# Kernel tuning notes

Measured on AMD Instinct MI355X. Metric: run time of the kernel, lower is better.

The kernel has to match this reference:

```python
import jax, jax.numpy as jnp
import numpy as np

B, C, J, T = 32, 128, 24, 128
Q, K = 6, 1024
EPS = 1e-10


def setup_inputs() -> dict:
    key = jax.random.key(0)
    k1, k2 = jax.random.split(key)
    x = jax.random.normal(k1, (B, C, J, T), dtype=jnp.float32)
    codebooks = jax.random.normal(k2, (Q, K, C), dtype=jnp.float32)
    return {"x": x, "codebooks": codebooks}


def reference(x, codebooks):
    """Residual VQ over 2D joint-temporal tokens.
    x: (B, C, J, T); codebooks: (Q, K, C).
    Returns (quantized_out (B,C,J,T), all_indices (B,J,T,Q), loss scalar, perplexity scalar).
    """
    b, c, j, t = x.shape
    q, k, _ = codebooks.shape
    # preprocess: (B, C, J, T) -> (B*J*T, C)
    xf = jnp.transpose(x, (0, 2, 3, 1)).reshape(-1, c)
    m = xf.shape[0]

    def step(carry, codebook):
        residual, q_out = carry
        # squared L2 distances (M, K)
        d = (jnp.sum(residual * residual, axis=-1, keepdims=True)
             - 2.0 * (residual @ codebook.T)
             + jnp.sum(codebook * codebook, axis=-1))
        idx = jnp.argmin(d, axis=-1)                       # (M,)
        xd = codebook[idx]                                 # dequantize (M, C)
        # commitment loss: mse(x, x_d.detach())
        loss = jnp.mean((residual - jax.lax.stop_gradient(xd)) ** 2)
        # perplexity from code usage histogram
        counts = jax.ops.segment_sum(jnp.ones((m,), xf.dtype), idx, num_segments=k)
        p = counts / m
        perp = jnp.exp(-jnp.sum(p * jnp.log(p + EPS)))
        # straight-through estimator
        quant = residual + jax.lax.stop_gradient(xd - residual)
        # residual = residual - quantized.detach(); quantized_out += quantized
        new_res = residual - jax.lax.stop_gradient(quant)
        return (new_res, q_out + quant), (idx, loss, perp)

    init = (xf, jnp.zeros_like(xf))
    (_, q_out), (idxs, losses, perps) = jax.lax.scan(step, init, codebooks)

    quantized_out = jnp.transpose(q_out.reshape(b, j, t, c), (0, 3, 1, 2))
    all_indices = jnp.transpose(idxs, (1, 0)).reshape(b, j, t, q)
    return quantized_out, all_indices, jnp.mean(losses), jnp.mean(perps)
```

## Files before the change

kernel.cpp:

```cpp
#include <hip/hip_runtime.h>

typedef __attribute__((ext_vector_type(8))) short short8v;
typedef __attribute__((ext_vector_type(4))) float f32x4;

#define B_ 32
#define C_ 128
#define J_ 24
#define T_ 128
#define Q_ 6
#define K_ 1024
#define JT (J_*T_)
#define M_ (B_*JT)
#define NBLK 768

#define OUT_QUANT 0
#define OUT_IDX   12582912
#define OUT_LOSS  13172736
#define OUT_PERP  13172737

#define TAU_S 0.01f

__device__ __forceinline__ unsigned short f2bf(float f) {
    unsigned int u = __float_as_uint(f);
    u = (u + 0x7FFFu + ((u >> 16) & 1u)) >> 16;
    return (unsigned short)u;
}
__device__ __forceinline__ float bf2f(unsigned short h) {
    return __uint_as_float(((unsigned int)h) << 16);
}

__device__ __forceinline__ void gload16(const void* g, void* lds) {
    __builtin_amdgcn_global_load_lds(
        (const __attribute__((address_space(1))) void*)g,
        (__attribute__((address_space(3))) void*)lds, 16, 0, 0);
}

__global__ __launch_bounds__(256) void c2_kernel(const float* __restrict__ cb,
                                                 float* __restrict__ c2) {
    int wave = (blockIdx.x * blockDim.x + threadIdx.x) >> 6;
    int lane = threadIdx.x & 63;
    if (wave >= Q_ * K_) return;
    const float2 v = reinterpret_cast<const float2*>(cb + (size_t)wave * C_)[lane];
    float s = v.x * v.x + v.y * v.y;
    #pragma unroll
    for (int off = 32; off; off >>= 1) s += __shfl_down(s, off, 64);
    if (lane == 0) c2[wave] = s;
}

__global__ __launch_bounds__(256) void cbtile_kernel(const float* __restrict__ cb,
                                                     unsigned short* __restrict__ cbt) {
    int i = blockIdx.x * 256 + threadIdx.x;
    if (i >= Q_ * 32 * 1024) return;
    int q = i >> 15;
    int rem = i & 32767;
    int tau = rem >> 10;
    int slot = rem & 1023;
    int part = slot >> 9;
    int ks = (slot >> 7) & 3;
    int nt = (slot >> 6) & 1;
    int r6 = slot & 63;
    int a = (r6 >> 4) & 3;
    int b3 = (r6 >> 3) & 1;
    int low3 = r6 & 7;
    int c4 = (b3 << 3) | (low3 ^ a);
    int code = tau * 32 + nt * 16 + c4;
    const float* src = cb + ((size_t)q * K_ + code) * C_ + ks * 32 + a * 8;
    short8v v;
    #pragma unroll
    for (int j = 0; j < 8; ++j) {
        float f = src[j];
        unsigned short hh = f2bf(f);
        v[j] = (part == 0) ? (short)hh : (short)f2bf(f - bf2f(hh));
    }
    *(short8v*)(cbt + (size_t)i * 8) = v;
}

__global__ __launch_bounds__(256) void transpose_kernel(const float* __restrict__ x,
                                                        float* __restrict__ res) {
    __shared__ float tile[32][33];
    const int tx = threadIdx.x & 31, ty = threadIdx.x >> 5;
    const int jt0 = blockIdx.x * 32;
    const int c0 = blockIdx.y * 32;
    const int b = blockIdx.z;
    const float* xb = x + ((size_t)b * C_ + c0) * JT + jt0;
    #pragma unroll
    for (int i = 0; i < 4; ++i) {
        int cc = ty + 8 * i;
        tile[cc][tx] = xb[(size_t)cc * JT + tx];
    }
    __syncthreads();
    float* rb = res + ((size_t)b * JT + jt0) * C_ + c0;
    #pragma unroll
    for (int i = 0; i < 4; ++i) {
        int jj = ty + 8 * i;
        rb[(size_t)jj * C_ + tx] = tile[tx][jj];
    }
}

__global__ __launch_bounds__(256, 3) void vq_fused_kernel(
        float* __restrict__ res,
        const float* __restrict__ cb,
        const unsigned short* __restrict__ cbt,
        const float* __restrict__ c2g,
        int* __restrict__ idxws, int* __restrict__ counts,
        float* __restrict__ partials) {
    __shared__ __attribute__((aligned(16))) unsigned short bsA[8192];
    __shared__ __attribute__((aligned(16))) unsigned short bsB[8192];
    __shared__ __attribute__((aligned(16))) unsigned short bsC[8192];
    __shared__ int idx_lds[128];
    __shared__ int nflag[4];
    __shared__ int flagl[4][32];
    __shared__ float wsum[4];
    __shared__ __attribute__((aligned(16))) float rowbuf[4][128];

    const int t = threadIdx.x;
    const int w = t >> 6, l = t & 63;
    const int la = l >> 4;
    const int lc = l & 15;
    const int rowbase = blockIdx.x * 128 + w * 32;
    const int lb = la * 256 + (l & 8) * 16 + (((l & 7) ^ la) * 16);

    float rres[64];
    #pragma unroll
    for (int mf = 0; mf < 2; ++mf) {
        const float* ap = res + (size_t)(rowbase + mf * 16 + lc) * C_ + la * 8;
        #pragma unroll
        for (int ks = 0; ks < 4; ++ks) {
            float4 f0 = *(const float4*)(ap + ks * 32);
            float4 f1 = *(const float4*)(ap + ks * 32 + 4);
            rres[mf * 32 + ks * 8 + 0] = f0.x; rres[mf * 32 + ks * 8 + 1] = f0.y;
            rres[mf * 32 + ks * 8 + 2] = f0.z; rres[mf * 32 + ks * 8 + 3] = f0.w;
            rres[mf * 32 + ks * 8 + 4] = f1.x; rres[mf * 32 + ks * 8 + 5] = f1.y;
            rres[mf * 32 + ks * 8 + 6] = f1.z; rres[mf * 32 + ks * 8 + 7] = f1.w;
        }
    }

#define STAGE(base_, tau_, buf_) { \
        const unsigned short* sp = (base_) + (size_t)(tau_) * 8192 + w * 2048 + l * 8; \
        char* dp = ((char*)(buf_)) + w * 4096; \
        gload16(sp, dp); \
        gload16(sp + 512, dp + 1024); \
        gload16(sp + 1024, dp + 2048); \
        gload16(sp + 1536, dp + 3072); \
    }

    for (int q = 0; q < Q_; ++q) {
        const int qk0 = q * K_;
        const unsigned short* cbase = cbt + (size_t)q * (32 * 8192);
        if (l == 0) nflag[w] = 0;

        float c2r0 = c2g[qk0 + lc];
        float c2r1 = c2g[qk0 + 16 + lc];

        STAGE(cbase, 0, bsA)
        STAGE(cbase, 1, bsB)

        short8v ah[2][4], al[2][4];
        #pragma unroll
        for (int mf = 0; mf < 2; ++mf) {
            #pragma unroll
            for (int ks = 0; ks < 4; ++ks) {
                short8v vh, vl;
                #pragma unroll
                for (int j = 0; j < 8; ++j) {
                    float v = rres[mf * 32 + ks * 8 + j];
                    unsigned short hh = f2bf(v);
                    vh[j] = (short)hh;
                    vl[j] = (short)f2bf(v - bf2f(hh));
                }
                ah[mf][ks] = vh;
                al[mf][ks] = vl;
            }
        }

        float bs[2][4], bs2[2][4];
        int bi[2][4];
        #pragma unroll
        for (int mf = 0; mf < 2; ++mf)
            #pragma unroll
            for (int rg = 0; rg < 4; ++rg) {
                bs[mf][rg] = -3.4e38f; bs2[mf][rg] = -3.4e38f; bi[mf][rg] = 0;
            }

        asm volatile("s_waitcnt vmcnt(4)" ::: "memory");
        __builtin_amdgcn_s_barrier();
        float c2n0 = -0.5f * c2r0;
        float c2n1 = -0.5f * c2r1;

        const char* bcur = (const char*)bsA;
        const char* bnx1 = (const char*)bsB;
        const char* bnx2 = (const char*)bsC;

        for (int tau = 0; tau < 32; ++tau) {
            if (tau < 31) {
                c2r0 = c2g[qk0 + (tau + 1) * 32 + lc];
                c2r1 = c2g[qk0 + (tau + 1) * 32 + 16 + lc];
            }
            if (tau < 30) STAGE(cbase, tau + 2, (void*)bnx2)

            #pragma unroll
            for (int nt = 0; nt < 2; ++nt) {
                const int code = tau * 32 + nt * 16 + lc;
                const float cinit = nt ? c2n1 : c2n0;
                f32x4 acc0 = {cinit, cinit, cinit, cinit};
                f32x4 acc1 = acc0;
                #pragma unroll
                for (int ks = 0; ks < 4; ++ks) {
                    const char* bb = bcur + ks * 2048 + nt * 1024 + lb;
                    const short8v bh = *(const short8v*)(bb);
                    const short8v bl = *(const short8v*)(bb + 8192);
                    acc0 = __builtin_amdgcn_mfma_f32_16x16x32_bf16(ah[0][ks], bh, acc0, 0, 0, 0);
                    acc0 = __builtin_amdgcn_mfma_f32_16x16x32_bf16(al[0][ks], bh, acc0, 0, 0, 0);
                    acc0 = __builtin_amdgcn_mfma_f32_16x16x32_bf16(ah[0][ks], bl, acc0, 0, 0, 0);
                    acc1 = __builtin_amdgcn_mfma_f32_16x16x32_bf16(ah[1][ks], bh, acc1, 0, 0, 0);
                    acc1 = __builtin_amdgcn_mfma_f32_16x16x32_bf16(al[1][ks], bh, acc1, 0, 0, 0);
                    acc1 = __builtin_amdgcn_mfma_f32_16x16x32_bf16(ah[1][ks], bl, acc1, 0, 0, 0);
                }
#define UPD(A, mf, rg) { \
                float v = A[rg]; \
                bs2[mf][rg] = fmaxf(bs2[mf][rg], fminf(bs[mf][rg], v)); \
                bool gt = v > bs[mf][rg]; \
                bs[mf][rg] = fmaxf(bs[mf][rg], v); \
                bi[mf][rg] = gt ? code : bi[mf][rg]; }
                UPD(acc0, 0, 0) UPD(acc0, 0, 1) UPD(acc0, 0, 2) UPD(acc0, 0, 3)
                UPD(acc1, 1, 0) UPD(acc1, 1, 1) UPD(acc1, 1, 2) UPD(acc1, 1, 3)
#undef UPD
            }

            if (tau < 30) {
                asm volatile("s_waitcnt vmcnt(4)" ::: "memory");
            } else if (tau == 30) {
                asm volatile("s_waitcnt vmcnt(2)" ::: "memory");
            } else {
                asm volatile("s_waitcnt vmcnt(0)" ::: "memory");
            }
            __builtin_amdgcn_s_barrier();
            c2n0 = -0.5f * c2r0;
            c2n1 = -0.5f * c2r1;
            const char* tmp = bcur; bcur = bnx1; bnx1 = bnx2; bnx2 = tmp;
        }

        #pragma unroll
        for (int mf = 0; mf < 2; ++mf) {
            #pragma unroll
            for (int rg = 0; rg < 4; ++rg) {
                float s1 = bs[mf][rg], s2 = bs2[mf][rg];
                int i1 = bi[mf][rg];
                #pragma unroll
                for (int off = 1; off < 16; off <<= 1) {
                    float os1 = __shfl_xor(s1, off);
                    float os2 = __shfl_xor(s2, off);
                    int oi1 = __shfl_xor(i1, off);
                    float ns2 = fmaxf(fmaxf(s2, os2), fminf(s1, os1));
                    if (os1 > s1 || (os1 == s1 && oi1 < i1)) { s1 = os1; i1 = oi1; }
                    s2 = ns2;
                }
                if (lc == 0) {
                    const int rr = mf * 16 + la * 4 + rg;
                    idx_lds[w * 32 + rr] = i1;
                    if (s1 - s2 < TAU_S) {
                        int p = atomicAdd(&nflag[w], 1);
                        flagl[w][p] = rr;
                    }
                }
            }
        }

        {
            const int nf = nflag[w];
            for (int f = 0; f < nf; ++f) {
                const int rr = flagl[w][f];
                const int mfr = rr >> 4, r16 = rr & 15;
                if (lc == r16) {
                    #pragma unroll
                    for (int ks = 0; ks < 4; ++ks) {
                        #pragma unroll
                        for (int j = 0; j < 8; ++j)
                            rowbuf[w][la * 8 + ks * 32 + j] =
                                (mfr == 0) ? rres[ks * 8 + j] : rres[32 + ks * 8 + j];
                    }
                }
                asm volatile("s_waitcnt lgkmcnt(0)" ::: "memory");
                __builtin_amdgcn_sched_barrier(0);
                const float4* rf4 = (const float4*)&rowbuf[w][0];
                double bdd = 1e300;
                int bk = 0;
                for (int kk = 0; kk < 16; ++kk) {
                    const int k = l + kk * 64;
                    const float4* bp4 = (const float4*)(cb + ((size_t)qk0 + k) * C_);
                    double s = 0.0;
                    for (int c4 = 0; c4 < 32; ++c4) {
                        float4 bv = bp4[c4];
                        float4 rv = rf4[c4];
                        double d0 = (double)rv.x - (double)bv.x; s = fma(d0, d0, s);
                        double d1 = (double)rv.y - (double)bv.y; s = fma(d1, d1, s);
                        double d2 = (double)rv.z - (double)bv.z; s = fma(d2, d2, s);
                        double d3 = (double)rv.w - (double)bv.w; s = fma(d3, d3, s);
                    }
                    if (s < bdd || (s == bdd && k < bk)) { bdd = s; bk = k; }
                }
                #pragma unroll
                for (int off = 1; off < 64; off <<= 1) {
                    double od = __shfl_xor(bdd, off);
                    int ok = __shfl_xor(bk, off);
                    if (od < bdd || (od == bdd && ok < bk)) { bdd = od; bk = ok; }
                }
                if (l == 0) idx_lds[w * 32 + rr] = bk;
                asm volatile("s_waitcnt lgkmcnt(0)" ::: "memory");
            }
        }

        if (l < 16) {
            const int k0 = idx_lds[w * 32 + l];
            const int k1 = idx_lds[w * 32 + 16 + l];
            idxws[(size_t)q * M_ + rowbase + l] = k0;
            idxws[(size_t)q * M_ + rowbase + 16 + l] = k1;
            atomicAdd(&counts[qk0 + k0], 1);
            atomicAdd(&counts[qk0 + k1], 1);
        }

        float sq = 0.f;
        #pragma unroll
        for (int mf = 0; mf < 2; ++mf) {
            const int k = idx_lds[w * 32 + mf * 16 + lc];
            const float* cbr = cb + ((size_t)qk0 + k) * C_ + la * 8;
            #pragma unroll
            for (int ks = 0; ks < 4; ++ks) {
                float4 cv0 = *(const float4*)(cbr + ks * 32);
                float4 cv1 = *(const float4*)(cbr + ks * 32 + 4);
                float cvv[8] = {cv0.x, cv0.y, cv0.z, cv0.w, cv1.x, cv1.y, cv1.z, cv1.w};
                #pragma unroll
                for (int j = 0; j < 8; ++j) {
                    float rv = rres[mf * 32 + ks * 8 + j];
                    float cvj = cvv[j];
                    float dd = rv - cvj;
                    sq += dd * dd;
                    rres[mf * 32 + ks * 8 + j] = rv - (rv + (cvj - rv));
                }
            }
        }
        #pragma unroll
        for (int off = 32; off; off >>= 1) sq += __shfl_down(sq, off, 64);
        if (l == 0) wsum[w] = sq;
        __syncthreads();
        if (t == 0) partials[q * NBLK + blockIdx.x] = wsum[0] + wsum[1] + wsum[2] + wsum[3];
        __syncthreads();
    }

    #pragma unroll
    for (int mf = 0; mf < 2; ++mf) {
        float* ap = res + (size_t)(rowbase + mf * 16 + lc) * C_ + la * 8;
        #pragma unroll
        for (int ks = 0; ks < 4; ++ks) {
            float4 f0 = *(const float4*)(ap + ks * 32);
            float4 f1 = *(const float4*)(ap + ks * 32 + 4);
            float4 o0, o1;
            o0.x = f0.x - rres[mf * 32 + ks * 8 + 0];
            o0.y = f0.y - rres[mf * 32 + ks * 8 + 1];
            o0.z = f0.z - rres[mf * 32 + ks * 8 + 2];
            o0.w = f0.w - rres[mf * 32 + ks * 8 + 3];
            o1.x = f1.x - rres[mf * 32 + ks * 8 + 4];
            o1.y = f1.y - rres[mf * 32 + ks * 8 + 5];
            o1.z = f1.z - rres[mf * 32 + ks * 8 + 6];
            o1.w = f1.w - rres[mf * 32 + ks * 8 + 7];
            *(float4*)(ap + ks * 32) = o0;
            *(float4*)(ap + ks * 32 + 4) = o1;
        }
    }
#undef STAGE
}

__global__ __launch_bounds__(256) void scalars_kernel(const float* __restrict__ partials,
                                                      const int* __restrict__ counts,
                                                      float* __restrict__ out) {
    __shared__ float red[256];
    const int t = threadIdx.x;
    float loss_acc = 0.f, perp_acc = 0.f;
    for (int q = 0; q < Q_; ++q) {
        float s = 0.f;
        for (int i = t; i < NBLK; i += 256) s += partials[q * NBLK + i];
        red[t] = s;
        __syncthreads();
        for (int o = 128; o; o >>= 1) {
            if (t < o) red[t] += red[t + o];
            __syncthreads();
        }
        if (t == 0) loss_acc += red[0] / (float)(M_ * C_);
        __syncthreads();
    }
    for (int q = 0; q < Q_; ++q) {
        float s = 0.f;
        for (int k = t; k < K_; k += 256) {
            float p = (float)counts[q * K_ + k] / (float)M_;
            s += p * logf(p + 1e-10f);
        }
        red[t] = s;
        __syncthreads();
        for (int o = 128; o; o >>= 1) {
            if (t < o) red[t] += red[t + o];
            __syncthreads();
        }
        if (t == 0) perp_acc += expf(-red[0]);
        __syncthreads();
    }
    if (t == 0) {
        out[OUT_LOSS] = loss_acc / (float)Q_;
        out[OUT_PERP] = perp_acc / (float)Q_;
    }
}

__global__ __launch_bounds__(256) void finalt_kernel(const float* __restrict__ qout,
                                                     float* __restrict__ out) {
    __shared__ float tile[32][33];
    const int tx = threadIdx.x & 31, ty = threadIdx.x >> 5;
    const int jt0 = blockIdx.x * 32;
    const int c0 = blockIdx.y * 32;
    const int b = blockIdx.z;
    const float* qb = qout + ((size_t)b * JT + jt0) * C_ + c0;
    #pragma unroll
    for (int i = 0; i < 4; ++i) {
        int jj = ty + 8 * i;
        tile[jj][tx] = qb[(size_t)jj * C_ + tx];
    }
    __syncthreads();
    float* ob = out + ((size_t)b * C_ + c0) * JT + jt0;
    #pragma unroll
    for (int i = 0; i < 4; ++i) {
        int cc = ty + 8 * i;
        ob[(size_t)cc * JT + tx] = tile[tx][cc];
    }
}

__global__ __launch_bounds__(256) void idxout_kernel(const int* __restrict__ idxin,
                                                     float* __restrict__ out) {
    int f = blockIdx.x * 256 + threadIdx.x;
    if (f >= M_ * Q_) return;
    int m = f / Q_;
    int q = f - m * Q_;
    out[f] = (float)idxin[q * M_ + m];
}

extern "C" void kernel_launch(void* const* d_in, const int* in_sizes, int n_in,
                              void* d_out, int out_size, void* d_ws, size_t ws_size,
                              hipStream_t stream) {
    const float* x = (const float*)d_in[0];
    const float* cb = (const float*)d_in[1];
    float* out = (float*)d_out;
    char* ws = (char*)d_ws;

    float* res = (float*)ws;
    int* idxws = (int*)(ws + 50331648);
    float* c2 = (float*)(ws + 52690944);
    int* counts = (int*)(ws + 52715520);
    float* partials = (float*)(ws + 52740096);
    unsigned short* cbt = (unsigned short*)(ws + 52758528);

    hipMemsetAsync(counts, 0, Q_ * K_ * sizeof(int), stream);
    c2_kernel<<<1536, 256, 0, stream>>>(cb, c2);
    cbtile_kernel<<<768, 256, 0, stream>>>(cb, cbt);
    transpose_kernel<<<dim3(96, 4, 32), 256, 0, stream>>>(x, res);
    vq_fused_kernel<<<NBLK, 256, 0, stream>>>(res, cb, cbt, c2, idxws, counts, partials);
    scalars_kernel<<<1, 256, 0, stream>>>(partials, counts, out);
    finalt_kernel<<<dim3(96, 4, 32), 256, 0, stream>>>(res, out);
    idxout_kernel<<<2304, 256, 0, stream>>>(idxws, out + OUT_IDX);
}
```

Baseline: 780.4 us.

## Halve rows per block and split MFMA accumulators into three independent chains

```diff
diff --git a/kernel.cpp b/kernel.cpp
--- a/kernel.cpp
+++ b/kernel.cpp
@@ -11,7 +11,7 @@
 #define K_ 1024
 #define JT (J_*T_)
 #define M_ (B_*JT)
-#define NBLK 768
+#define NBLK 1536
 
 #define OUT_QUANT 0
 #define OUT_IDX   12582912
@@ -97,7 +97,7 @@
     }
 }
 
-__global__ __launch_bounds__(256, 3) void vq_fused_kernel(
+__global__ __launch_bounds__(256, 2) void vq_fused_kernel(
         float* __restrict__ res,
         const float* __restrict__ cb,
         const unsigned short* __restrict__ cbt,
@@ -107,9 +107,9 @@
     __shared__ __attribute__((aligned(16))) unsigned short bsA[8192];
     __shared__ __attribute__((aligned(16))) unsigned short bsB[8192];
     __shared__ __attribute__((aligned(16))) unsigned short bsC[8192];
-    __shared__ int idx_lds[128];
+    __shared__ int idx_lds[64];
     __shared__ int nflag[4];
-    __shared__ int flagl[4][32];
+    __shared__ int flagl[4][16];
     __shared__ float wsum[4];
     __shared__ __attribute__((aligned(16))) float rowbuf[4][128];
 
@@ -117,21 +117,20 @@
     const int w = t >> 6, l = t & 63;
     const int la = l >> 4;
     const int lc = l & 15;
-    const int rowbase = blockIdx.x * 128 + w * 32;
+    const int rowbase = blockIdx.x * 64 + w * 16;
     const int lb = la * 256 + (l & 8) * 16 + (((l & 7) ^ la) * 16);
 
-    float rres[64];
-    #pragma unroll
-    for (int mf = 0; mf < 2; ++mf) {
-        const float* ap = res + (size_t)(rowbase + mf * 16 + lc) * C_ + la * 8;
+    float rres[32];
+    {
+        const float* ap = res + (size_t)(rowbase + lc) * C_ + la * 8;
         #pragma unroll
         for (int ks = 0; ks < 4; ++ks) {
             float4 f0 = *(const float4*)(ap + ks * 32);
             float4 f1 = *(const float4*)(ap + ks * 32 + 4);
-            rres[mf * 32 + ks * 8 + 0] = f0.x; rres[mf * 32 + ks * 8 + 1] = f0.y;
-            rres[mf * 32 + ks * 8 + 2] = f0.z; rres[mf * 32 + ks * 8 + 3] = f0.w;
-            rres[mf * 32 + ks * 8 + 4] = f1.x; rres[mf * 32 + ks * 8 + 5] = f1.y;
-            rres[mf * 32 + ks * 8 + 6] = f1.z; rres[mf * 32 + ks * 8 + 7] = f1.w;
+            rres[ks * 8 + 0] = f0.x; rres[ks * 8 + 1] = f0.y;
+            rres[ks * 8 + 2] = f0.z; rres[ks * 8 + 3] = f0.w;
+            rres[ks * 8 + 4] = f1.x; rres[ks * 8 + 5] = f1.y;
+            rres[ks * 8 + 6] = f1.z; rres[ks * 8 + 7] = f1.w;
         }
     }
 
@@ -155,32 +154,27 @@
         STAGE(cbase, 0, bsA)
         STAGE(cbase, 1, bsB)
 
-        short8v ah[2][4], al[2][4];
-        #pragma unroll
-        for (int mf = 0; mf < 2; ++mf) {
+        short8v ah[4], al[4];
+        #pragma unroll
+        for (int ks = 0; ks < 4; ++ks) {
+            short8v vh, vl;
             #pragma unroll
-            for (int ks = 0; ks < 4; ++ks) {
-                short8v vh, vl;
-                #pragma unroll
-                for (int j = 0; j < 8; ++j) {
-                    float v = rres[mf * 32 + ks * 8 + j];
-                    unsigned short hh = f2bf(v);
-                    vh[j] = (short)hh;
-                    vl[j] = (short)f2bf(v - bf2f(hh));
-                }
-                ah[mf][ks] = vh;
-                al[mf][ks] = vl;
-            }
-        }
-
-        float bs[2][4], bs2[2][4];
-        int bi[2][4];
-        #pragma unroll
-        for (int mf = 0; mf < 2; ++mf)
-            #pragma unroll
-            for (int rg = 0; rg < 4; ++rg) {
-                bs[mf][rg] = -3.4e38f; bs2[mf][rg] = -3.4e38f; bi[mf][rg] = 0;
-            }
+            for (int j = 0; j < 8; ++j) {
+                float v = rres[ks * 8 + j];
+                unsigned short hh = f2bf(v);
+                vh[j] = (short)hh;
+                vl[j] = (short)f2bf(v - bf2f(hh));
+            }
+            ah[ks] = vh;
+            al[ks] = vl;
+        }
+
+        float bsv[4], bs2[4];
+        int bi[4];
+        #pragma unroll
+        for (int rg = 0; rg < 4; ++rg) {
+            bsv[rg] = -3.4e38f; bs2[rg] = -3.4e38f; bi[rg] = 0;
+        }
 
         asm volatile("s_waitcnt vmcnt(4)" ::: "memory");
         __builtin_amdgcn_s_barrier();
@@ -202,28 +196,25 @@
             for (int nt = 0; nt < 2; ++nt) {
                 const int code = tau * 32 + nt * 16 + lc;
                 const float cinit = nt ? c2n1 : c2n0;
-                f32x4 acc0 = {cinit, cinit, cinit, cinit};
-                f32x4 acc1 = acc0;
+                f32x4 aA = {cinit, cinit, cinit, cinit};
+                f32x4 aB = {0.f, 0.f, 0.f, 0.f};
+                f32x4 aC = {0.f, 0.f, 0.f, 0.f};
                 #pragma unroll
                 for (int ks = 0; ks < 4; ++ks) {
                     const char* bb = bcur + ks * 2048 + nt * 1024 + lb;
                     const short8v bh = *(const short8v*)(bb);
                     const short8v bl = *(const short8v*)(bb + 8192);
-                    acc0 = __builtin_amdgcn_mfma_f32_16x16x32_bf16(ah[0][ks], bh, acc0, 0, 0, 0);
-                    acc0 = __builtin_amdgcn_mfma_f32_16x16x32_bf16(al[0][ks], bh, acc0, 0, 0, 0);
-                    acc0 = __builtin_amdgcn_mfma_f32_16x16x32_bf16(ah[0][ks], bl, acc0, 0, 0, 0);
-                    acc1 = __builtin_amdgcn_mfma_f32_16x16x32_bf16(ah[1][ks], bh, acc1, 0, 0, 0);
-                    acc1 = __builtin_amdgcn_mfma_f32_16x16x32_bf16(al[1][ks], bh, acc1, 0, 0, 0);
-                    acc1 = __builtin_amdgcn_mfma_f32_16x16x32_bf16(ah[1][ks], bl, acc1, 0, 0, 0);
-                }
-#define UPD(A, mf, rg) { \
-                float v = A[rg]; \
-                bs2[mf][rg] = fmaxf(bs2[mf][rg], fminf(bs[mf][rg], v)); \
-                bool gt = v > bs[mf][rg]; \
-                bs[mf][rg] = fmaxf(bs[mf][rg], v); \
-                bi[mf][rg] = gt ? code : bi[mf][rg]; }
-                UPD(acc0, 0, 0) UPD(acc0, 0, 1) UPD(acc0, 0, 2) UPD(acc0, 0, 3)
-                UPD(acc1, 1, 0) UPD(acc1, 1, 1) UPD(acc1, 1, 2) UPD(acc1, 1, 3)
+                    aA = __builtin_amdgcn_mfma_f32_16x16x32_bf16(ah[ks], bh, aA, 0, 0, 0);
+                    aB = __builtin_amdgcn_mfma_f32_16x16x32_bf16(al[ks], bh, aB, 0, 0, 0);
+                    aC = __builtin_amdgcn_mfma_f32_16x16x32_bf16(ah[ks], bl, aC, 0, 0, 0);
+                }
+#define UPD(rg) { \
+                float v = (aA[rg] + aB[rg]) + aC[rg]; \
+                bs2[rg] = fmaxf(bs2[rg], fminf(bsv[rg], v)); \
+                bool gt = v > bsv[rg]; \
+                bsv[rg] = fmaxf(bsv[rg], v); \
+                bi[rg] = gt ? code : bi[rg]; }
+                UPD(0) UPD(1) UPD(2) UPD(3)
 #undef UPD
             }
 
@@ -241,27 +232,24 @@
         }
 
         #pragma unroll
-        for (int mf = 0; mf < 2; ++mf) {
+        for (int rg = 0; rg < 4; ++rg) {
+            float s1 = bsv[rg], s2 = bs2[rg];
+            int i1 = bi[rg];
             #pragma unroll
-            for (int rg = 0; rg < 4; ++rg) {
-                float s1 = bs[mf][rg], s2 = bs2[mf][rg];
-                int i1 = bi[mf][rg];
-                #pragma unroll
-                for (int off = 1; off < 16; off <<= 1) {
-                    float os1 = __shfl_xor(s1, off);
-                    float os2 = __shfl_xor(s2, off);
-                    int oi1 = __shfl_xor(i1, off);
-                    float ns2 = fmaxf(fmaxf(s2, os2), fminf(s1, os1));
-                    if (os1 > s1 || (os1 == s1 && oi1 < i1)) { s1 = os1; i1 = oi1; }
-                    s2 = ns2;
-                }
-                if (lc == 0) {
-                    const int rr = mf * 16 + la * 4 + rg;
-                    idx_lds[w * 32 + rr] = i1;
-                    if (s1 - s2 < TAU_S) {
-                        int p = atomicAdd(&nflag[w], 1);
-                        flagl[w][p] = rr;
-                    }
+            for (int off = 1; off < 16; off <<= 1) {
+                float os1 = __shfl_xor(s1, off);
+                float os2 = __shfl_xor(s2, off);
+                int oi1 = __shfl_xor(i1, off);
+                float ns2 = fmaxf(fmaxf(s2, os2), fminf(s1, os1));
+                if (os1 > s1 || (os1 == s1 && oi1 < i1)) { s1 = os1; i1 = oi1; }
+                s2 = ns2;
+            }
+            if (lc == 0) {
+                const int rr = la * 4 + rg;
+                idx_lds[w * 16 + rr] = i1;
+                if (s1 - s2 < TAU_S) {
+                    int p = atomicAdd(&nflag[w], 1);
+                    flagl[w][p] = rr;
                 }
             }
         }
@@ -270,14 +258,12 @@
             const int nf = nflag[w];
             for (int f = 0; f < nf; ++f) {
                 const int rr = flagl[w][f];
-                const int mfr = rr >> 4, r16 = rr & 15;
-                if (lc == r16) {
+                if (lc == rr) {
                     #pragma unroll
                     for (int ks = 0; ks < 4; ++ks) {
                         #pragma unroll
                         for (int j = 0; j < 8; ++j)
-                            rowbuf[w][la * 8 + ks * 32 + j] =
-                                (mfr == 0) ? rres[ks * 8 + j] : rres[32 + ks * 8 + j];
+                            rowbuf[w][la * 8 + ks * 32 + j] = rres[ks * 8 + j];
                     }
                 }
                 asm volatile("s_waitcnt lgkmcnt(0)" ::: "memory");
@@ -305,24 +291,20 @@
                     int ok = __shfl_xor(bk, off);
                     if (od < bdd || (od == bdd && ok < bk)) { bdd = od; bk = ok; }
                 }
-                if (l == 0) idx_lds[w * 32 + rr] = bk;
+                if (l == 0) idx_lds[w * 16 + rr] = bk;
                 asm volatile("s_waitcnt lgkmcnt(0)" ::: "memory");
             }
         }
 
         if (l < 16) {
-            const int k0 = idx_lds[w * 32 + l];
-            const int k1 = idx_lds[w * 32 + 16 + l];
+            const int k0 = idx_lds[w * 16 + l];
             idxws[(size_t)q * M_ + rowbase + l] = k0;
-            idxws[(size_t)q * M_ + rowbase + 16 + l] = k1;
             atomicAdd(&counts[qk0 + k0], 1);
-            atomicAdd(&counts[qk0 + k1], 1);
         }
 
         float sq = 0.f;
-        #pragma unroll
-        for (int mf = 0; mf < 2; ++mf) {
-            const int k = idx_lds[w * 32 + mf * 16 + lc];
+        {
+            const int k = idx_lds[w * 16 + lc];
             const float* cbr = cb + ((size_t)qk0 + k) * C_ + la * 8;
             #pragma unroll
             for (int ks = 0; ks < 4; ++ks) {
@@ -331,11 +313,11 @@
                 float cvv[8] = {cv0.x, cv0.y, cv0.z, cv0.w, cv1.x, cv1.y, cv1.z, cv1.w};
                 #pragma unroll
                 for (int j = 0; j < 8; ++j) {
-                    float rv = rres[mf * 32 + ks * 8 + j];
+                    float rv = rres[ks * 8 + j];
                     float cvj = cvv[j];
                     float dd = rv - cvj;
                     sq += dd * dd;
-                    rres[mf * 32 + ks * 8 + j] = rv - (rv + (cvj - rv));
+                    rres[ks * 8 + j] = rv - (rv + (cvj - rv));
                 }
             }
         }
@@ -347,22 +329,21 @@
         __syncthreads();
     }
 
-    #pragma unroll
-    for (int mf = 0; mf < 2; ++mf) {
-        float* ap = res + (size_t)(rowbase + mf * 16 + lc) * C_ + la * 8;
+    {
+        float* ap = res + (size_t)(rowbase + lc) * C_ + la * 8;
         #pragma unroll
         for (int ks = 0; ks < 4; ++ks) {
             float4 f0 = *(const float4*)(ap + ks * 32);
             float4 f1 = *(const float4*)(ap + ks * 32 + 4);
             float4 o0, o1;
-            o0.x = f0.x - rres[mf * 32 + ks * 8 + 0];
-            o0.y = f0.y - rres[mf * 32 + ks * 8 + 1];
-            o0.z = f0.z - rres[mf * 32 + ks * 8 + 2];
-            o0.w = f0.w - rres[mf * 32 + ks * 8 + 3];
-            o1.x = f1.x - rres[mf * 32 + ks * 8 + 4];
-            o1.y = f1.y - rres[mf * 32 + ks * 8 + 5];
-            o1.z = f1.z - rres[mf * 32 + ks * 8 + 6];
-            o1.w = f1.w - rres[mf * 32 + ks * 8 + 7];
+            o0.x = f0.x - rres[ks * 8 + 0];
+            o0.y = f0.y - rres[ks * 8 + 1];
+            o0.z = f0.z - rres[ks * 8 + 2];
+            o0.w = f0.w - rres[ks * 8 + 3];
+            o1.x = f1.x - rres[ks * 8 + 4];
+            o1.y = f1.y - rres[ks * 8 + 5];
+            o1.z = f1.z - rres[ks * 8 + 6];
+            o1.w = f1.w - rres[ks * 8 + 7];
             *(float4*)(ap + ks * 32) = o0;
             *(float4*)(ap + ks * 32 + 4) = o1;
         }
@@ -453,7 +434,7 @@
     float* c2 = (float*)(ws + 52690944);
     int* counts = (int*)(ws + 52715520);
     float* partials = (float*)(ws + 52740096);
-    unsigned short* cbt = (unsigned short*)(ws + 52758528);
+    unsigned short* cbt = (unsigned short*)(ws + 52776960);
 
     hipMemsetAsync(counts, 0, Q_ * K_ * sizeof(int), stream);
     c2_kernel<<<1536, 256, 0, stream>>>(cb, c2);
```

Result: slower. 952.8 us (+22.1%).
